# Kernel tuning notes

Measured on AMD Instinct MI355X. Metric: run time of the kernel, lower is better.

## Reference

```python
import jax, jax.numpy as jnp
import numpy as np

N = 100000          # number of nodes (queries == sources here)
DEG = 32            # uniform neighbor count
E = N * DEG         # total edges
C_IN = 8
HID = 32
C_OUT = 32


def setup_inputs() -> dict:
    key = jax.random.key(0)
    k1, k2, k3, k4, k5 = jax.random.split(key, 5)
    in_features = jax.random.normal(k1, (N, C_IN), dtype=jnp.float32)
    in_weights = jax.random.uniform(k2, (N,), dtype=jnp.float32)
    # MLP: Linear(2*C_IN -> HID), GELU, Linear(HID -> C_OUT)
    W1 = jax.random.normal(k3, (2 * C_IN, HID), dtype=jnp.float32) / np.sqrt(2 * C_IN)
    b1 = jnp.zeros((HID,), dtype=jnp.float32)
    W2 = jax.random.normal(k4, (HID, C_OUT), dtype=jnp.float32) / np.sqrt(HID)
    b2 = jnp.zeros((C_OUT,), dtype=jnp.float32)
    neighbor_index = jax.random.randint(k5, (E,), 0, N, dtype=jnp.int64)
    row_splits = (jnp.arange(N + 1, dtype=jnp.int64) * DEG)  # uniform CSR splits
    return {"in_features": in_features, "in_weights": in_weights,
            "W1": W1, "b1": b1, "W2": W2, "b2": b2,
            "neighbor_index": neighbor_index, "row_splits": row_splits}


def reference(in_features, in_weights, W1, b1, W2, b2, neighbor_index, row_splits):
    num_edges = neighbor_index.shape[0]
    num_out = row_splits.shape[0] - 1  # M output nodes
    # segment id of each edge (== repeat_interleave of node ids by row counts)
    seg = jnp.searchsorted(row_splits, jnp.arange(num_edges), side="right") - 1
    gathered = in_features[neighbor_index]          # [E, C_in] neighbor gather
    self_feats = in_features[seg]                   # [E, C_in] repeated self features
    agg = jnp.concatenate([gathered, self_feats], axis=1)  # [E, 2*C_in]
    h = jax.nn.gelu(agg @ W1 + b1)                  # [E, HID]
    h = h @ W2 + b2                                 # [E, C_out]
    h = in_weights[neighbor_index][:, None] * h     # quadrature weighting
    sums = jax.ops.segment_sum(h, seg, num_segments=num_out)  # segment_csr sum
    counts = (row_splits[1:] - row_splits[:-1]).astype(h.dtype)
    out = sums / jnp.maximum(counts, 1)[:, None]    # reduce='mean'
    return out
```

## Files before the change

### kernel.cpp

```cpp
#include <hip/hip_runtime.h>

#define DEG 32
#define HID 32
#define CIN 8

typedef float v2f __attribute__((ext_vector_type(2)));
typedef short bf16x8 __attribute__((ext_vector_type(8)));
typedef float f32x16 __attribute__((ext_vector_type(16)));

#define GELU_A ((float)(2.0 * 1.4426950408889634 * 0.7978845608028654))
#define GELU_B ((float)(2.0 * 1.4426950408889634 * 0.7978845608028654 * 0.044715))

__device__ __forceinline__ unsigned f2bf(float f) {
    unsigned b = __float_as_uint(f);
    return (b + 0x7fffu + ((b >> 16) & 1u)) >> 16;
}
__device__ __forceinline__ unsigned pack2(float lo, float hi) {
    return f2bf(lo) | (f2bf(hi) << 16);
}

__global__ __launch_bounds__(256) void precompute_xw(
    const float* __restrict__ x, const float* __restrict__ W1,
    unsigned* __restrict__ x16, unsigned* __restrict__ w1f, int N) {
    int tid = blockIdx.x * 256 + threadIdx.x;
    if (blockIdx.x == 0 && threadIdx.x < 64) {
        int l  = threadIdx.x;
        int kb = (l >> 5) * 8;
        int col = l & 31;
        uint4 o;
        o.x = pack2(W1[(kb + 0) * HID + col], W1[(kb + 1) * HID + col]);
        o.y = pack2(W1[(kb + 2) * HID + col], W1[(kb + 3) * HID + col]);
        o.z = pack2(W1[(kb + 4) * HID + col], W1[(kb + 5) * HID + col]);
        o.w = pack2(W1[(kb + 6) * HID + col], W1[(kb + 7) * HID + col]);
        *(uint4*)(w1f + l * 4) = o;
    }
    if (tid < N) {
        const float4* xp = (const float4*)(x + (size_t)tid * CIN);
        float4 a = xp[0], b = xp[1];
        uint4 o;
        o.x = pack2(a.x, a.y);  o.y = pack2(a.z, a.w);
        o.z = pack2(b.x, b.y);  o.w = pack2(b.z, b.w);
        *(uint4*)(x16 + (size_t)tid * 4) = o;
    }
}

__global__ __launch_bounds__(256) void git_mfma(
    const unsigned* __restrict__ x16, const unsigned* __restrict__ w1f,
    const float* __restrict__ wgt, const float* __restrict__ b1,
    const float* __restrict__ W2, const float* __restrict__ b2,
    const int* __restrict__ nbr, float* __restrict__ out, int N) {
    __shared__ float sW2[HID * HID];
    __shared__ float sw[4 * DEG];
    __shared__ float sg[4 * HID];

    int t = threadIdx.x;
#pragma unroll
    for (int i = 0; i < 4; ++i) sW2[t + i * 256] = W2[t + i * 256];

    int wv = t >> 6;
    int l  = t & 63;
    int l5 = l & 31;
    int hi = l >> 5;
    int node = blockIdx.x * 4 + wv;
    int nc = node < N ? node : (N - 1);

    int   jn = nbr[nc * DEG + l5];
    float w  = wgt[jn];
    if (hi == 0) sw[wv * DEG + l5] = w;

    float ws = w;
    ws += __shfl_xor(ws, 1);  ws += __shfl_xor(ws, 2);
    ws += __shfl_xor(ws, 4);  ws += __shfl_xor(ws, 8);
    ws += __shfl_xor(ws, 16);

    int arow = hi ? nc : jn;
    bf16x8 af = *((const bf16x8*)x16 + arow);
    bf16x8 bf = *((const bf16x8*)w1f + l);
    float myb1 = b1[l5];

    f32x16 acc = {};
    acc = __builtin_amdgcn_mfma_f32_32x32x16_bf16(af, bf, acc, 0, 0, 0);

    int base = hi * 4;
    const float* swp = &sw[wv * DEG + base];
    float4 wq0 = *(const float4*)(swp);
    float4 wq1 = *(const float4*)(swp + 8);
    float4 wq2 = *(const float4*)(swp + 16);
    float4 wq3 = *(const float4*)(swp + 24);
    float wqa[16] = {wq0.x, wq0.y, wq0.z, wq0.w,  wq1.x, wq1.y, wq1.z, wq1.w,
                     wq2.x, wq2.y, wq2.z, wq2.w,  wq3.x, wq3.y, wq3.z, wq3.w};

    float g = 0.f;
#pragma unroll
    for (int i = 0; i < 16; i += 2) {
        v2f tt = {acc[i] + myb1, acc[i + 1] + myb1};
        v2f x2 = tt * tt;
        v2f zz = tt * (x2 * GELU_B + GELU_A);
        v2f ee;
        ee.x = __builtin_amdgcn_exp2f(zz.x);  ee.y = __builtin_amdgcn_exp2f(zz.y);
        v2f dd = ee + 1.0f;
        v2f rr;
        rr.x = __builtin_amdgcn_rcpf(dd.x);   rr.y = __builtin_amdgcn_rcpf(dd.y);
        v2f gl = tt - tt * rr;
        g = fmaf(wqa[i],     gl.x, g);
        g = fmaf(wqa[i + 1], gl.y, g);
    }
    g += __shfl_xor(g, 32);
    if (hi == 0) sg[wv * HID + l5] = g;

    __syncthreads();

    const float* gp  = &sg[wv * HID + hi * 16];
    const float* w2p = &sW2[(hi * 16) * HID + l5];
    float4 g0 = *(const float4*)(gp);
    float4 g1 = *(const float4*)(gp + 4);
    float4 g2 = *(const float4*)(gp + 8);
    float4 g3 = *(const float4*)(gp + 12);
    float ga[16] = {g0.x, g0.y, g0.z, g0.w,  g1.x, g1.y, g1.z, g1.w,
                    g2.x, g2.y, g2.z, g2.w,  g3.x, g3.y, g3.z, g3.w};
    float acc2 = 0.f;
#pragma unroll
    for (int h = 0; h < 16; ++h)
        acc2 = fmaf(ga[h], w2p[h * HID], acc2);
    acc2 += __shfl_xor(acc2, 32);

    if (node < N && hi == 0)
        out[(size_t)node * HID + l5] = fmaf(ws, b2[l5], acc2) * (1.0f / DEG);
}

__global__ __launch_bounds__(256) void fused_fallback(
    const float* __restrict__ x, const float* __restrict__ wgt,
    const float* __restrict__ W1, const float* __restrict__ b1,
    const float* __restrict__ W2, const float* __restrict__ b2,
    const int* __restrict__ nbr, float* __restrict__ out, int N) {
    __shared__ float sW2[HID * HID];
    __shared__ float sb2[HID];
    __shared__ int2  sp[8 * DEG];
    int t = threadIdx.x;
#pragma unroll
    for (int i = 0; i < 4; ++i) sW2[t + i * 256] = W2[t + i * 256];
    if (t < HID) sb2[t] = b2[t];
    int slot = t >> 5, hid = t & 31;
    int node = blockIdx.x * 8 + slot;
    bool valid = node < N;
    int nc = valid ? node : (N - 1);
    int   j_own = nbr[nc * DEG + hid];
    float w_own = wgt[j_own];
    sp[slot * DEG + hid] = make_int2(j_own * (CIN * 4), __float_as_int(w_own));
    const float4* xip = (const float4*)(x + (size_t)nc * CIN);
    float4 xa = xip[0], xb = xip[1];
    float w1t[8];
#pragma unroll
    for (int k = 0; k < 8; ++k) w1t[k] = W1[k * HID + hid];
    float vb = b1[hid];
    vb = fmaf(xa.x, W1[ 8 * HID + hid], vb);
    vb = fmaf(xa.y, W1[ 9 * HID + hid], vb);
    vb = fmaf(xa.z, W1[10 * HID + hid], vb);
    vb = fmaf(xa.w, W1[11 * HID + hid], vb);
    vb = fmaf(xb.x, W1[12 * HID + hid], vb);
    vb = fmaf(xb.y, W1[13 * HID + hid], vb);
    vb = fmaf(xb.z, W1[14 * HID + hid], vb);
    vb = fmaf(xb.w, W1[15 * HID + hid], vb);
    float ws = w_own;
    ws += __shfl_xor(ws, 1);  ws += __shfl_xor(ws, 2);
    ws += __shfl_xor(ws, 4);  ws += __shfl_xor(ws, 8);
    ws += __shfl_xor(ws, 16);
    __syncthreads();
    const char* xbytes = (const char*)x;
    const int2* myp = &sp[slot * DEG];
    float g = 0.f;
#pragma unroll 8
    for (int e = 0; e < DEG; ++e) {
        int2  p  = myp[e];
        float wjv = __int_as_float(p.y);
        const float4* xjp = (const float4*)(xbytes + (unsigned)p.x);
        float4 a = xjp[0], b = xjp[1];
        float tin = vb;
        tin = fmaf(a.x, w1t[0], tin); tin = fmaf(a.y, w1t[1], tin);
        tin = fmaf(a.z, w1t[2], tin); tin = fmaf(a.w, w1t[3], tin);
        tin = fmaf(b.x, w1t[4], tin); tin = fmaf(b.y, w1t[5], tin);
        tin = fmaf(b.z, w1t[6], tin); tin = fmaf(b.w, w1t[7], tin);
        float x2 = tin * tin;
        float z  = tin * fmaf(GELU_B, x2, GELU_A);
        float e2 = __builtin_amdgcn_exp2f(z);
        float r  = __builtin_amdgcn_rcpf(1.0f + e2);
        g = fmaf(wjv, fmaf(-tin, r, tin), g);
    }
    float acc = 0.f;
#pragma unroll
    for (int h = 0; h < HID; ++h) {
        float gh = __shfl(g, h, 32);
        acc = fmaf(gh, sW2[h * HID + hid], acc);
    }
    if (valid) out[(size_t)node * HID + hid] = fmaf(ws, sb2[hid], acc) * (1.0f / DEG);
}

extern "C" void kernel_launch(void* const* d_in, const int* in_sizes, int n_in,
                              void* d_out, int out_size, void* d_ws, size_t ws_size,
                              hipStream_t stream) {
    const float* x   = (const float*)d_in[0];
    const float* wq  = (const float*)d_in[1];
    const float* W1  = (const float*)d_in[2];
    const float* b1  = (const float*)d_in[3];
    const float* W2  = (const float*)d_in[4];
    const float* b2  = (const float*)d_in[5];
    const int*   nbr = (const int*)d_in[6];
    float* out = (float*)d_out;

    int N = in_sizes[1];
    size_t need = (size_t)N * 16 + 1024;

    if (ws_size >= need) {
        unsigned* x16 = (unsigned*)d_ws;
        unsigned* w1f = (unsigned*)((char*)d_ws + (size_t)N * 16);
        int blocks_pre = (N + 255) / 256;
        precompute_xw<<<blocks_pre, 256, 0, stream>>>(x, W1, x16, w1f, N);
        int blocks_main = (N + 3) / 4;
        git_mfma<<<blocks_main, 256, 0, stream>>>(x16, w1f, wq, b1, W2, b2, nbr, out, N);
    } else {
        int blocks = (N + 7) / 8;
        fused_fallback<<<blocks, 256, 0, stream>>>(x, wq, W1, b1, W2, b2, nbr, out, N);
    }
}
```

Measured before the change: 117.4 us.

## Split W2 projection into separate bf16 MFMA epilogue kernel over node tiles

Moves the per-node HID×C_OUT projection out of the main kernel into a new epilogue kernel that runs 32-node tiles through bf16 MFMA. The main kernel writes the weighted GELU sums as bf16 plus a per-node weight sum, which removes the W2 shared-memory load, the __syncthreads and the scalar FMA loop. It also folds b1 into the accumulator init and rewrites GELU as t*sigmoid. The cost is an extra kernel launch, a round trip of intermediates through global memory, and bf16 rounding of g before the second matmul.

```diff
diff --git a/kernel.cpp b/kernel.cpp
--- a/kernel.cpp
+++ b/kernel.cpp
@@ -21,18 +21,30 @@
 
 __global__ __launch_bounds__(256) void precompute_xw(
     const float* __restrict__ x, const float* __restrict__ W1,
-    unsigned* __restrict__ x16, unsigned* __restrict__ w1f, int N) {
+    const float* __restrict__ W2, unsigned* __restrict__ x16,
+    unsigned* __restrict__ w1f, unsigned* __restrict__ w2f, int N) {
     int tid = blockIdx.x * 256 + threadIdx.x;
-    if (blockIdx.x == 0 && threadIdx.x < 64) {
-        int l  = threadIdx.x;
-        int kb = (l >> 5) * 8;
-        int col = l & 31;
-        uint4 o;
-        o.x = pack2(W1[(kb + 0) * HID + col], W1[(kb + 1) * HID + col]);
-        o.y = pack2(W1[(kb + 2) * HID + col], W1[(kb + 3) * HID + col]);
-        o.z = pack2(W1[(kb + 4) * HID + col], W1[(kb + 5) * HID + col]);
-        o.w = pack2(W1[(kb + 6) * HID + col], W1[(kb + 7) * HID + col]);
-        *(uint4*)(w1f + l * 4) = o;
+    if (blockIdx.x == 0) {
+        int t = threadIdx.x;
+        if (t < 64) {
+            int kb = (t >> 5) * 8, col = t & 31;
+            uint4 o;
+            o.x = pack2(W1[(kb + 0) * HID + col], W1[(kb + 1) * HID + col]);
+            o.y = pack2(W1[(kb + 2) * HID + col], W1[(kb + 3) * HID + col]);
+            o.z = pack2(W1[(kb + 4) * HID + col], W1[(kb + 5) * HID + col]);
+            o.w = pack2(W1[(kb + 6) * HID + col], W1[(kb + 7) * HID + col]);
+            *(uint4*)(w1f + t * 4) = o;
+        } else if (t < 192) {
+            int u = t - 64;
+            int f = u >> 6, l = u & 63;
+            int kb = f * 16 + ((l >> 5) * 8), col = l & 31;
+            uint4 o;
+            o.x = pack2(W2[(kb + 0) * HID + col], W2[(kb + 1) * HID + col]);
+            o.y = pack2(W2[(kb + 2) * HID + col], W2[(kb + 3) * HID + col]);
+            o.z = pack2(W2[(kb + 4) * HID + col], W2[(kb + 5) * HID + col]);
+            o.w = pack2(W2[(kb + 6) * HID + col], W2[(kb + 7) * HID + col]);
+            *(uint4*)(w2f + (f * 64 + l) * 4) = o;
+        }
     }
     if (tid < N) {
         const float4* xp = (const float4*)(x + (size_t)tid * CIN);
@@ -44,19 +56,14 @@
     }
 }
 
-__global__ __launch_bounds__(256) void git_mfma(
+__global__ __launch_bounds__(256) void git_core(
     const unsigned* __restrict__ x16, const unsigned* __restrict__ w1f,
     const float* __restrict__ wgt, const float* __restrict__ b1,
-    const float* __restrict__ W2, const float* __restrict__ b2,
-    const int* __restrict__ nbr, float* __restrict__ out, int N) {
-    __shared__ float sW2[HID * HID];
+    const int* __restrict__ nbr, unsigned short* __restrict__ g16,
+    float* __restrict__ wsum, int N) {
     __shared__ float sw[4 * DEG];
-    __shared__ float sg[4 * HID];
 
     int t = threadIdx.x;
-#pragma unroll
-    for (int i = 0; i < 4; ++i) sW2[t + i * 256] = W2[t + i * 256];
-
     int wv = t >> 6;
     int l  = t & 63;
     int l5 = l & 31;
@@ -78,11 +85,12 @@
     bf16x8 bf = *((const bf16x8*)w1f + l);
     float myb1 = b1[l5];
 
-    f32x16 acc = {};
+    f32x16 acc;
+#pragma unroll
+    for (int i = 0; i < 16; ++i) acc[i] = myb1;
     acc = __builtin_amdgcn_mfma_f32_32x32x16_bf16(af, bf, acc, 0, 0, 0);
 
-    int base = hi * 4;
-    const float* swp = &sw[wv * DEG + base];
+    const float* swp = &sw[wv * DEG + hi * 4];
     float4 wq0 = *(const float4*)(swp);
     float4 wq1 = *(const float4*)(swp + 8);
     float4 wq2 = *(const float4*)(swp + 16);
@@ -90,42 +98,78 @@
     float wqa[16] = {wq0.x, wq0.y, wq0.z, wq0.w,  wq1.x, wq1.y, wq1.z, wq1.w,
                      wq2.x, wq2.y, wq2.z, wq2.w,  wq3.x, wq3.y, wq3.z, wq3.w};
 
-    float g = 0.f;
+    v2f gacc = {0.f, 0.f};
 #pragma unroll
     for (int i = 0; i < 16; i += 2) {
-        v2f tt = {acc[i] + myb1, acc[i + 1] + myb1};
+        v2f tt = {acc[i], acc[i + 1]};
         v2f x2 = tt * tt;
-        v2f zz = tt * (x2 * GELU_B + GELU_A);
+        v2f zz = tt * (x2 * (-GELU_B) + (-GELU_A));
         v2f ee;
         ee.x = __builtin_amdgcn_exp2f(zz.x);  ee.y = __builtin_amdgcn_exp2f(zz.y);
         v2f dd = ee + 1.0f;
         v2f rr;
         rr.x = __builtin_amdgcn_rcpf(dd.x);   rr.y = __builtin_amdgcn_rcpf(dd.y);
-        v2f gl = tt - tt * rr;
-        g = fmaf(wqa[i],     gl.x, g);
-        g = fmaf(wqa[i + 1], gl.y, g);
-    }
+        v2f wp = {wqa[i], wqa[i + 1]};
+        gacc += wp * (tt * rr);
+    }
+    float g = gacc.x + gacc.y;
     g += __shfl_xor(g, 32);
-    if (hi == 0) sg[wv * HID + l5] = g;
-
-    __syncthreads();
-
-    const float* gp  = &sg[wv * HID + hi * 16];
-    const float* w2p = &sW2[(hi * 16) * HID + l5];
-    float4 g0 = *(const float4*)(gp);
-    float4 g1 = *(const float4*)(gp + 4);
-    float4 g2 = *(const float4*)(gp + 8);
-    float4 g3 = *(const float4*)(gp + 12);
-    float ga[16] = {g0.x, g0.y, g0.z, g0.w,  g1.x, g1.y, g1.z, g1.w,
-                    g2.x, g2.y, g2.z, g2.w,  g3.x, g3.y, g3.z, g3.w};
-    float acc2 = 0.f;
-#pragma unroll
-    for (int h = 0; h < 16; ++h)
-        acc2 = fmaf(ga[h], w2p[h * HID], acc2);
-    acc2 += __shfl_xor(acc2, 32);
-
-    if (node < N && hi == 0)
-        out[(size_t)node * HID + l5] = fmaf(ws, b2[l5], acc2) * (1.0f / DEG);
+
+    if (node < N && hi == 0) {
+        g16[(size_t)node * HID + l5] = (unsigned short)f2bf(g);
+        if (l5 == 0) wsum[node] = ws;
+    }
+}
+
+__global__ __launch_bounds__(256) void epilogue_mfma(
+    const unsigned short* __restrict__ g16, const unsigned* __restrict__ w2f,
+    const float* __restrict__ wsum, const float* __restrict__ b2,
+    float* __restrict__ out, int N) {
+    int t = threadIdx.x;
+    int wv = t >> 6;
+    int l  = t & 63;
+    int l5 = l & 31;
+    int hi = l >> 5;
+    int tile = blockIdx.x * 4 + wv;
+    int ntiles = (N + 31) >> 5;
+    if (tile >= ntiles) return;
+    int nb = tile * 32;
+
+    int row = nb + l5;  if (row >= N) row = N - 1;
+    bf16x8 a1 = *(const bf16x8*)(g16 + (size_t)row * HID + hi * 8);
+    bf16x8 a2 = *(const bf16x8*)(g16 + (size_t)row * HID + 16 + hi * 8);
+    bf16x8 bf1 = *((const bf16x8*)w2f + l);
+    bf16x8 bf2 = *((const bf16x8*)w2f + 64 + l);
+
+    f32x16 acc = {};
+    acc = __builtin_amdgcn_mfma_f32_32x32x16_bf16(a1, bf1, acc, 0, 0, 0);
+    acc = __builtin_amdgcn_mfma_f32_32x32x16_bf16(a2, bf2, acc, 0, 0, 0);
+
+    float myb2 = b2[l5];
+    float wsa[16];
+    if (nb + 32 <= N) {
+        const float* wp = wsum + nb + hi * 4;
+        float4 q0 = *(const float4*)(wp);
+        float4 q1 = *(const float4*)(wp + 8);
+        float4 q2 = *(const float4*)(wp + 16);
+        float4 q3 = *(const float4*)(wp + 24);
+        wsa[0]=q0.x; wsa[1]=q0.y; wsa[2]=q0.z; wsa[3]=q0.w;
+        wsa[4]=q1.x; wsa[5]=q1.y; wsa[6]=q1.z; wsa[7]=q1.w;
+        wsa[8]=q2.x; wsa[9]=q2.y; wsa[10]=q2.z; wsa[11]=q2.w;
+        wsa[12]=q3.x; wsa[13]=q3.y; wsa[14]=q3.z; wsa[15]=q3.w;
+    } else {
+#pragma unroll
+        for (int i = 0; i < 16; ++i) {
+            int r = nb + (i & 3) + 8 * (i >> 2) + 4 * hi;
+            wsa[i] = wsum[r < N ? r : (N - 1)];
+        }
+    }
+#pragma unroll
+    for (int i = 0; i < 16; ++i) {
+        int r = nb + (i & 3) + 8 * (i >> 2) + 4 * hi;
+        if (r < N)
+            out[(size_t)r * HID + l5] = fmaf(wsa[i], myb2, acc[i]) * (1.0f / DEG);
+    }
 }
 
 __global__ __launch_bounds__(256) void fused_fallback(
@@ -208,15 +252,30 @@
     float* out = (float*)d_out;
 
     int N = in_sizes[1];
-    size_t need = (size_t)N * 16 + 1024;
+
+    size_t off_x16 = 0;
+    size_t off_g16 = (off_x16 + (size_t)N * 16 + 255) & ~(size_t)255;
+    size_t off_ws  = (off_g16 + (size_t)N * 64 + 255) & ~(size_t)255;
+    size_t off_w1  = (off_ws  + (size_t)N * 4  + 255) & ~(size_t)255;
+    size_t off_w2  = off_w1 + 1024;
+    size_t need    = off_w2 + 2048;
 
     if (ws_size >= need) {
-        unsigned* x16 = (unsigned*)d_ws;
-        unsigned* w1f = (unsigned*)((char*)d_ws + (size_t)N * 16);
+        unsigned*       x16  = (unsigned*)((char*)d_ws + off_x16);
+        unsigned short* g16p = (unsigned short*)((char*)d_ws + off_g16);
+        float*          wsum = (float*)((char*)d_ws + off_ws);
+        unsigned*       w1f  = (unsigned*)((char*)d_ws + off_w1);
+        unsigned*       w2f  = (unsigned*)((char*)d_ws + off_w2);
+
         int blocks_pre = (N + 255) / 256;
-        precompute_xw<<<blocks_pre, 256, 0, stream>>>(x, W1, x16, w1f, N);
+        precompute_xw<<<blocks_pre, 256, 0, stream>>>(x, W1, W2, x16, w1f, w2f, N);
+
         int blocks_main = (N + 3) / 4;
-        git_mfma<<<blocks_main, 256, 0, stream>>>(x16, w1f, wq, b1, W2, b2, nbr, out, N);
+        git_core<<<blocks_main, 256, 0, stream>>>(x16, w1f, wq, b1, nbr, g16p, wsum, N);
+
+        int ntiles = (N + 31) / 32;
+        int blocks_epi = (ntiles + 3) / 4;
+        epilogue_mfma<<<blocks_epi, 256, 0, stream>>>(g16p, w2f, wsum, b2, out, N);
     } else {
         int blocks = (N + 7) / 8;
         fused_fallback<<<blocks, 256, 0, stream>>>(x, wq, W1, b1, W2, b2, nbr, out, N);
```

Result: slower. 121.4 us (+3.4%).
